# Performance work log

Hardware: AMD Instinct MI355X
Metric: run time of the kernel (lower is better)

## Reference

```python
import jax, jax.numpy as jnp
import numpy as np

N_NODES = 100000


def setup_inputs() -> dict:
    key = jax.random.key(0)
    ks = jax.random.split(key, 7)
    N, F, C, K, E = N_NODES, 64, 32, 3, 1_600_000
    x = jax.random.normal(ks[0], (N, F), dtype=jnp.float32)
    edge_vals = jax.random.uniform(ks[1], (K, E), dtype=jnp.float32)
    W = jax.random.normal(ks[2], (F, C), dtype=jnp.float32) / np.sqrt(F)
    b = jax.random.normal(ks[3], (C,), dtype=jnp.float32) * 0.01
    alpha = jnp.ones((K,), dtype=jnp.float32)
    edge_rows = jax.random.randint(ks[4], (K, E), 0, N, dtype=jnp.int64 if jax.config.jax_enable_x64 else jnp.int32)
    edge_cols = jax.random.randint(ks[5], (K, E), 0, N, dtype=jnp.int64 if jax.config.jax_enable_x64 else jnp.int32)
    return {"x": x, "edge_vals": edge_vals, "W": W, "b": b, "alpha": alpha,
            "edge_rows": edge_rows, "edge_cols": edge_cols}


def reference(x, edge_vals, W, b, alpha, edge_rows, edge_cols):
    # Fused form of: (sum_k alpha[k] * A_k) @ x, then Linear.
    # Per hop k: agg_k[n] = sum_{e: rows[k,e]==n} vals[k,e] * x[cols[k,e]]
    def hop_spmm(vals, rows, cols):
        msg = vals[:, None] * x[cols]                      # [E, F] gather + scale
        return jax.ops.segment_sum(msg, rows, num_segments=N_NODES)  # [N, F]

    agg = jax.vmap(hop_spmm)(edge_vals, edge_rows, edge_cols)  # [K, N, F]
    h = jnp.einsum('k,knf->nf', alpha, agg)                    # weighted hop sum
    return h @ W + b                                           # [N, C]
```

## Files before the change

kernel.cpp:

```cpp
#include <hip/hip_runtime.h>

#define N_NODES 100000
#define F 64
#define C 32
#define KH 3
#define E 1600000
#define NE (KH * E)

#define NSLICE 4
#define SLICEW 25000
#define NKEY (N_NODES * NSLICE)
#define KPB 512
#define NBUCK ((NKEY + KPB - 1) / KPB)
#define CHUNK 4096
#define NCHUNK ((NE + CHUNK - 1) / CHUNK)
#define P2CAP 8192

__global__ __launch_bounds__(256) void gemm_xw(const float* __restrict__ x,
                                               const float* __restrict__ W,
                                               float* __restrict__ y) {
    __shared__ float Ws[F * C];
    for (int i = threadIdx.x; i < F * C; i += 256) Ws[i] = W[i];
    __syncthreads();

    const int g = blockIdx.x * 256 + threadIdx.x;
    if (g >= N_NODES * 2) return;
    const int node = g >> 1;
    const int h = (g & 1) * 16;

    const float4* xp = (const float4*)(x + (size_t)node * F);
    float acc[16];
#pragma unroll
    for (int c = 0; c < 16; c++) acc[c] = 0.f;

#pragma unroll
    for (int i = 0; i < 16; i++) {
        float4 v = xp[i];
        const int f = i * 4;
#pragma unroll
        for (int c = 0; c < 16; c++) {
            acc[c] += v.x * Ws[(f + 0) * C + h + c];
            acc[c] += v.y * Ws[(f + 1) * C + h + c];
            acc[c] += v.z * Ws[(f + 2) * C + h + c];
            acc[c] += v.w * Ws[(f + 3) * C + h + c];
        }
    }

    float4* yo = (float4*)(y + (size_t)node * C + h);
#pragma unroll
    for (int i = 0; i < 4; i++)
        yo[i] = make_float4(acc[4 * i], acc[4 * i + 1], acc[4 * i + 2], acc[4 * i + 3]);
}

__global__ __launch_bounds__(256) void hist_c(const int* __restrict__ rows,
                                              int* __restrict__ hcnt) {
    __shared__ int hh[NBUCK];
    for (int i = threadIdx.x; i < NBUCK; i += 256) hh[i] = 0;
    __syncthreads();
    const int base = blockIdx.x * CHUNK;
#pragma unroll
    for (int j = 0; j < 4; j++) {
        const int e = base + j * 1024 + threadIdx.x * 4;
        if (e + 3 < NE) {
            const int4 r4 = *(const int4*)(rows + e);
            atomicAdd(&hh[r4.x >> 7], 1);
            atomicAdd(&hh[r4.y >> 7], 1);
            atomicAdd(&hh[r4.z >> 7], 1);
            atomicAdd(&hh[r4.w >> 7], 1);
        }
    }
    __syncthreads();
    for (int i = threadIdx.x; i < NBUCK; i += 256) {
        const int cc = hh[i];
        if (cc) atomicAdd(&hcnt[i], cc);
    }
}

__global__ __launch_bounds__(256) void scan_c(const int* __restrict__ hcnt,
                                              int* __restrict__ bstart,
                                              int* __restrict__ bcur,
                                              int* __restrict__ rs_start) {
    __shared__ int sA[1024], sB[1024];
    const int tid = threadIdx.x;
    for (int i = tid; i < 1024; i += 256) sA[i] = (i < NBUCK) ? hcnt[i] : 0;
    __syncthreads();
    int* src = sA;
    int* dst = sB;
    for (int d = 1; d < 1024; d <<= 1) {
        for (int i = tid; i < 1024; i += 256) {
            int v = src[i];
            if (i >= d) v += src[i - d];
            dst[i] = v;
        }
        __syncthreads();
        int* t = src; src = dst; dst = t;
    }
    for (int i = tid; i < NBUCK; i += 256) {
        const int excl = (i == 0) ? 0 : src[i - 1];
        bstart[i] = excl;
        bcur[i] = excl;
    }
    if (tid == 0) {
        bstart[NBUCK] = NE;
        rs_start[NKEY] = NE;
    }
}

__global__ __launch_bounds__(256) void part1_k(const float* __restrict__ vals,
                                               const int* __restrict__ rows,
                                               const int* __restrict__ cols,
                                               const float* __restrict__ alpha,
                                               int* __restrict__ bcur,
                                               int2* __restrict__ edgebuf) {
    __shared__ int sA[1024];
    __shared__ int wtot[4];
    __shared__ int lpos[NBUCK];
    __shared__ int lbase[NBUCK];
    __shared__ int2 stage[CHUNK];
    __shared__ unsigned short sbin[CHUNK];

    const int tid = threadIdx.x;
    const int base = blockIdx.x * CHUNK;

    for (int i = tid; i < 1024; i += 256) sA[i] = 0;
    __syncthreads();

    int kj[16], cj[16];
    float wj[16];
#pragma unroll
    for (int j = 0; j < 4; j++) {
        const int e = base + j * 1024 + tid * 4;
        if (e + 3 < NE) {
            const int4   r4 = *(const int4*)(rows + e);
            const int4   c4 = *(const int4*)(cols + e);
            const float4 v4 = *(const float4*)(vals + e);
            const float ak = alpha[(e >= 2 * E) ? 2 : (e >= E) ? 1 : 0];
            kj[j * 4 + 0] = r4.x * NSLICE + c4.x / SLICEW; cj[j * 4 + 0] = c4.x; wj[j * 4 + 0] = v4.x * ak;
            kj[j * 4 + 1] = r4.y * NSLICE + c4.y / SLICEW; cj[j * 4 + 1] = c4.y; wj[j * 4 + 1] = v4.y * ak;
            kj[j * 4 + 2] = r4.z * NSLICE + c4.z / SLICEW; cj[j * 4 + 2] = c4.z; wj[j * 4 + 2] = v4.z * ak;
            kj[j * 4 + 3] = r4.w * NSLICE + c4.w / SLICEW; cj[j * 4 + 3] = c4.w; wj[j * 4 + 3] = v4.w * ak;
            atomicAdd(&sA[kj[j * 4 + 0] >> 9], 1);
            atomicAdd(&sA[kj[j * 4 + 1] >> 9], 1);
            atomicAdd(&sA[kj[j * 4 + 2] >> 9], 1);
            atomicAdd(&sA[kj[j * 4 + 3] >> 9], 1);
        } else {
            kj[j * 4 + 0] = kj[j * 4 + 1] = kj[j * 4 + 2] = kj[j * 4 + 3] = -1;
        }
    }
    __syncthreads();

    {
        const int lane = tid & 63;
        const int w = tid >> 6;
        const int b4 = tid * 4;
        const int a0 = sA[b4], a1 = sA[b4 + 1], a2 = sA[b4 + 2], a3 = sA[b4 + 3];
        const int l1 = a0 + a1, l2 = l1 + a2, l3 = l2 + a3;
        int sc = l3;
#pragma unroll
        for (int d = 1; d < 64; d <<= 1) {
            int u = __shfl_up(sc, d);
            if (lane >= d) sc += u;
        }
        if (lane == 63) wtot[w] = sc;
        __syncthreads();
        int wb = 0;
#pragma unroll
        for (int q = 0; q < 4; q++)
            if (q < w) wb += wtot[q];
        const int tb = wb + sc - l3;
        sA[b4] = tb + a0; sA[b4 + 1] = tb + l1; sA[b4 + 2] = tb + l2; sA[b4 + 3] = tb + l3;
    }
    __syncthreads();

    for (int i = tid; i < NBUCK; i += 256) {
        const int excl = (i == 0) ? 0 : sA[i - 1];
        const int cnt = sA[i] - excl;
        lpos[i] = excl;
        if (cnt) lbase[i] = atomicAdd(&bcur[i], cnt);
    }
    __syncthreads();

#pragma unroll
    for (int j = 0; j < 16; j++) {
        if (kj[j] >= 0) {
            const int b = kj[j] >> 9;
            const int p = atomicAdd(&lpos[b], 1);
            stage[p] = make_int2(((kj[j] & (KPB - 1)) << 17) | cj[j],
                                 __float_as_int(wj[j]));
            sbin[p] = (unsigned short)b;
        }
    }
    __syncthreads();

    const int total = sA[1023];
    for (int p = tid; p < total; p += 256) {
        const int b = sbin[p];
        const int excl = (b == 0) ? 0 : sA[b - 1];
        edgebuf[lbase[b] + (p - excl)] = stage[p];
    }
}

__global__ __launch_bounds__(512) void part2_k(const int* __restrict__ bstart,
                                               int* __restrict__ rs_start,
                                               int2* __restrict__ edgebuf) {
    __shared__ int2 sstage[P2CAP];
    __shared__ int sh[KPB];
    __shared__ int sg[KPB];
    __shared__ int wtot[8];
    __shared__ int lbin[KPB];

    const int tid = threadIdx.x;
    const int b = blockIdx.x;
    const int bs = bstart[b];
    const int be = bstart[b + 1];
    const int n = be - bs;

    for (int k = tid; k < KPB; k += 512) sh[k] = 0;
    __syncthreads();

    if (n <= P2CAP) {
        for (int i = tid; i < n; i += 512) {
            const int2 e = edgebuf[bs + i];
            sstage[i] = e;
            atomicAdd(&sh[((unsigned)e.x) >> 17], 1);
        }
    }
    __syncthreads();

    {
        const int lane = tid & 63;
        const int w = tid >> 6;
        const int a0 = sh[tid];
        int sc = a0;
#pragma unroll
        for (int d = 1; d < 64; d <<= 1) {
            int u = __shfl_up(sc, d);
            if (lane >= d) sc += u;
        }
        if (lane == 63) wtot[w] = sc;
        __syncthreads();
        int wb = 0;
#pragma unroll
        for (int q = 0; q < 8; q++)
            if (q < w) wb += wtot[q];
        sg[tid] = wb + sc;
    }
    __syncthreads();

    for (int k = tid; k < KPB; k += 512) {
        const int st = bs + ((k == 0) ? 0 : sg[k - 1]);
        lbin[k] = st;
        const int idx = (b << 9) + k;
        if (idx < NKEY) rs_start[idx] = st;
    }
    __syncthreads();

    if (n > P2CAP) return;

    for (int i = tid; i < n; i += 512) {
        const int2 e = sstage[i];
        const int sub = ((unsigned)e.x) >> 17;
        const int pos = atomicAdd(&lbin[sub], 1);
        edgebuf[pos] = e;
    }
}

__global__ __launch_bounds__(256) void gathers9_k(const long long* __restrict__ eb,
                                                  const int* __restrict__ rs_start,
                                                  const float* __restrict__ y,
                                                  const float* __restrict__ bias,
                                                  float* __restrict__ out) {
    const int blk = blockIdx.x;
    const int s = blk & (NSLICE - 1);
    const int row = (blk >> 2) * 8 + (threadIdx.x >> 5);
    const int c = threadIdx.x & 31;
    const int key = row * NSLICE + s;
    const int st = rs_start[key];
    const int en = rs_start[key + 1];

    float acc = (s == 0) ? bias[c] : 0.f;

    int i = st;
    for (; i + 8 <= en; i += 8) {
        const long long l0 = __builtin_nontemporal_load(&eb[i + 0]);
        const long long l1 = __builtin_nontemporal_load(&eb[i + 1]);
        const long long l2 = __builtin_nontemporal_load(&eb[i + 2]);
        const long long l3 = __builtin_nontemporal_load(&eb[i + 3]);
        const long long l4 = __builtin_nontemporal_load(&eb[i + 4]);
        const long long l5 = __builtin_nontemporal_load(&eb[i + 5]);
        const long long l6 = __builtin_nontemporal_load(&eb[i + 6]);
        const long long l7 = __builtin_nontemporal_load(&eb[i + 7]);
        const float y0 = y[(((int)l0) & 0x1FFFF) * C + c];
        const float y1 = y[(((int)l1) & 0x1FFFF) * C + c];
        const float y2 = y[(((int)l2) & 0x1FFFF) * C + c];
        const float y3 = y[(((int)l3) & 0x1FFFF) * C + c];
        const float y4 = y[(((int)l4) & 0x1FFFF) * C + c];
        const float y5 = y[(((int)l5) & 0x1FFFF) * C + c];
        const float y6 = y[(((int)l6) & 0x1FFFF) * C + c];
        const float y7 = y[(((int)l7) & 0x1FFFF) * C + c];
        acc += __int_as_float((int)(l0 >> 32)) * y0;
        acc += __int_as_float((int)(l1 >> 32)) * y1;
        acc += __int_as_float((int)(l2 >> 32)) * y2;
        acc += __int_as_float((int)(l3 >> 32)) * y3;
        acc += __int_as_float((int)(l4 >> 32)) * y4;
        acc += __int_as_float((int)(l5 >> 32)) * y5;
        acc += __int_as_float((int)(l6 >> 32)) * y6;
        acc += __int_as_float((int)(l7 >> 32)) * y7;
    }
    for (; i + 4 <= en; i += 4) {
        const long long l0 = __builtin_nontemporal_load(&eb[i + 0]);
        const long long l1 = __builtin_nontemporal_load(&eb[i + 1]);
        const long long l2 = __builtin_nontemporal_load(&eb[i + 2]);
        const long long l3 = __builtin_nontemporal_load(&eb[i + 3]);
        const float y0 = y[(((int)l0) & 0x1FFFF) * C + c];
        const float y1 = y[(((int)l1) & 0x1FFFF) * C + c];
        const float y2 = y[(((int)l2) & 0x1FFFF) * C + c];
        const float y3 = y[(((int)l3) & 0x1FFFF) * C + c];
        acc += __int_as_float((int)(l0 >> 32)) * y0;
        acc += __int_as_float((int)(l1 >> 32)) * y1;
        acc += __int_as_float((int)(l2 >> 32)) * y2;
        acc += __int_as_float((int)(l3 >> 32)) * y3;
    }
    for (; i < en; i++) {
        const long long l0 = __builtin_nontemporal_load(&eb[i]);
        acc += __int_as_float((int)(l0 >> 32)) * y[(((int)l0) & 0x1FFFF) * C + c];
    }

    unsafeAtomicAdd(out + (size_t)row * C + c, acc);
}

__global__ __launch_bounds__(256) void scatter_edges(
    const float* __restrict__ vals, const int* __restrict__ rows,
    const int* __restrict__ cols, const float* __restrict__ alpha,
    const float* __restrict__ y, float* __restrict__ out_acc) {
    const int t = blockIdx.x * 256 + threadIdx.x;
    const int e = t >> 5;
    const int c = t & 31;
    if (e >= KH * E) return;
    const int k = (e >= 2 * E) ? 2 : (e >= E) ? 1 : 0;
    const float w = vals[e] * alpha[k];
    const float yv = y[(size_t)cols[e] * C + c];
    unsafeAtomicAdd(out_acc + (size_t)rows[e] * C + c, w * yv);
}

__global__ __launch_bounds__(256) void finalize_k(float* __restrict__ out,
                                                  const float* __restrict__ bias) {
    const int idx = (blockIdx.x * 256 + threadIdx.x) * 4;
    if (idx >= N_NODES * C) return;
    const int c0 = idx & (C - 1);
    float4 v = *(float4*)(out + idx);
    v.x += bias[c0 + 0];
    v.y += bias[c0 + 1];
    v.z += bias[c0 + 2];
    v.w += bias[c0 + 3];
    *(float4*)(out + idx) = v;
}

extern "C" void kernel_launch(void* const* d_in, const int* in_sizes, int n_in,
                              void* d_out, int out_size, void* d_ws, size_t ws_size,
                              hipStream_t stream) {
    const float* x         = (const float*)d_in[0];
    const float* edge_vals = (const float*)d_in[1];
    const float* W         = (const float*)d_in[2];
    const float* b         = (const float*)d_in[3];
    const float* alpha     = (const float*)d_in[4];
    const int*   edge_rows = (const int*)d_in[5];
    const int*   edge_cols = (const int*)d_in[6];
    float*       out       = (float*)d_out;

    const size_t offY   = 0;
    const size_t offEB  = (size_t)N_NODES * C * 4;
    const size_t offRS  = offEB + (size_t)NE * 8;
    const size_t offBS  = offRS + (((size_t)(NKEY + 1) * 4 + 255) & ~(size_t)255);
    const size_t offBC  = offBS + (((NBUCK + 1) * 4 + 255) & ~(size_t)255);
    const size_t offHC  = offBC + ((NBUCK * 4 + 255) & ~(size_t)255);
    const size_t need   = offHC + (size_t)NBUCK * 4;

    float* y = (float*)((char*)d_ws + offY);

    gemm_xw<<<(N_NODES * 2 + 255) / 256, 256, 0, stream>>>(x, W, y);

    if (ws_size >= need) {
        int2* edgebuf  = (int2*)((char*)d_ws + offEB);
        int*  rs_start = (int*)((char*)d_ws + offRS);
        int*  bstart   = (int*)((char*)d_ws + offBS);
        int*  bcur     = (int*)((char*)d_ws + offBC);
        int*  hcnt     = (int*)((char*)d_ws + offHC);

        hipMemsetAsync(hcnt, 0, (size_t)NBUCK * 4, stream);
        hipMemsetAsync(out, 0, (size_t)N_NODES * C * sizeof(float), stream);

        hist_c<<<NCHUNK, 256, 0, stream>>>(edge_rows, hcnt);
        scan_c<<<1, 256, 0, stream>>>(hcnt, bstart, bcur, rs_start);
        part1_k<<<NCHUNK, 256, 0, stream>>>(edge_vals, edge_rows, edge_cols,
                                            alpha, bcur, edgebuf);
        part2_k<<<NBUCK, 512, 0, stream>>>(bstart, rs_start, edgebuf);
        gathers9_k<<<(N_NODES / 8) * NSLICE, 256, 0, stream>>>(
            (const long long*)edgebuf, rs_start, y, b, out);
    } else {
        hipMemsetAsync(out, 0, (size_t)N_NODES * C * sizeof(float), stream);
        const long long scatter_threads = (long long)KH * E * C;
        const int scatter_blocks = (int)((scatter_threads + 255) / 256);
        scatter_edges<<<scatter_blocks, 256, 0, stream>>>(
            edge_vals, edge_rows, edge_cols, alpha, y, out);
        finalize_k<<<(N_NODES * C / 4 + 255) / 256, 256, 0, stream>>>(out, b);
    }
}
```

Baseline: 378.6 us.

## Fuse GEMM with row histogram launch and double partition chunk size

The x@W GEMM and the row-bucket histogram are merged into one kernel, with blocks split by index range, so the two independent passes overlap and one launch is removed. The first partition kernel now processes 8192-edge chunks with 512 threads instead of 4096 with 256. This halves the number of global bucket-cursor atomics and makes the write-out runs per bucket longer. The larger shared staging buffer (about 90KB) limits the kernel to fewer resident blocks per CU.

```diff
diff --git a/kernel.cpp b/kernel.cpp
--- a/kernel.cpp
+++ b/kernel.cpp
@@ -12,67 +12,73 @@
 #define NKEY (N_NODES * NSLICE)
 #define KPB 512
 #define NBUCK ((NKEY + KPB - 1) / KPB)
-#define CHUNK 4096
-#define NCHUNK ((NE + CHUNK - 1) / CHUNK)
+#define HCHUNK 4096
+#define NHCHUNK ((NE + HCHUNK - 1) / HCHUNK)
+#define CHUNK1 8192
+#define NCHUNK1 ((NE + CHUNK1 - 1) / CHUNK1)
 #define P2CAP 8192
-
-__global__ __launch_bounds__(256) void gemm_xw(const float* __restrict__ x,
-                                               const float* __restrict__ W,
-                                               float* __restrict__ y) {
-    __shared__ float Ws[F * C];
-    for (int i = threadIdx.x; i < F * C; i += 256) Ws[i] = W[i];
-    __syncthreads();
-
-    const int g = blockIdx.x * 256 + threadIdx.x;
-    if (g >= N_NODES * 2) return;
-    const int node = g >> 1;
-    const int h = (g & 1) * 16;
-
-    const float4* xp = (const float4*)(x + (size_t)node * F);
-    float acc[16];
-#pragma unroll
-    for (int c = 0; c < 16; c++) acc[c] = 0.f;
-
-#pragma unroll
-    for (int i = 0; i < 16; i++) {
-        float4 v = xp[i];
-        const int f = i * 4;
-#pragma unroll
-        for (int c = 0; c < 16; c++) {
-            acc[c] += v.x * Ws[(f + 0) * C + h + c];
-            acc[c] += v.y * Ws[(f + 1) * C + h + c];
-            acc[c] += v.z * Ws[(f + 2) * C + h + c];
-            acc[c] += v.w * Ws[(f + 3) * C + h + c];
-        }
-    }
-
-    float4* yo = (float4*)(y + (size_t)node * C + h);
-#pragma unroll
-    for (int i = 0; i < 4; i++)
-        yo[i] = make_float4(acc[4 * i], acc[4 * i + 1], acc[4 * i + 2], acc[4 * i + 3]);
-}
-
-__global__ __launch_bounds__(256) void hist_c(const int* __restrict__ rows,
-                                              int* __restrict__ hcnt) {
-    __shared__ int hh[NBUCK];
-    for (int i = threadIdx.x; i < NBUCK; i += 256) hh[i] = 0;
-    __syncthreads();
-    const int base = blockIdx.x * CHUNK;
-#pragma unroll
-    for (int j = 0; j < 4; j++) {
-        const int e = base + j * 1024 + threadIdx.x * 4;
-        if (e + 3 < NE) {
-            const int4 r4 = *(const int4*)(rows + e);
-            atomicAdd(&hh[r4.x >> 7], 1);
-            atomicAdd(&hh[r4.y >> 7], 1);
-            atomicAdd(&hh[r4.z >> 7], 1);
-            atomicAdd(&hh[r4.w >> 7], 1);
-        }
-    }
-    __syncthreads();
-    for (int i = threadIdx.x; i < NBUCK; i += 256) {
-        const int cc = hh[i];
-        if (cc) atomicAdd(&hcnt[i], cc);
+#define GEMM_BLOCKS ((N_NODES * 2 + 255) / 256)
+
+__global__ __launch_bounds__(256) void gemm_hist_k(const float* __restrict__ x,
+                                                   const float* __restrict__ W,
+                                                   float* __restrict__ y,
+                                                   const int* __restrict__ rows,
+                                                   int* __restrict__ hcnt) {
+    __shared__ float smem[F * C];
+
+    if (blockIdx.x < GEMM_BLOCKS) {
+        float* Ws = smem;
+        for (int i = threadIdx.x; i < F * C; i += 256) Ws[i] = W[i];
+        __syncthreads();
+
+        const int g = blockIdx.x * 256 + threadIdx.x;
+        if (g >= N_NODES * 2) return;
+        const int node = g >> 1;
+        const int h = (g & 1) * 16;
+
+        const float4* xp = (const float4*)(x + (size_t)node * F);
+        float acc[16];
+#pragma unroll
+        for (int c = 0; c < 16; c++) acc[c] = 0.f;
+
+#pragma unroll
+        for (int i = 0; i < 16; i++) {
+            float4 v = xp[i];
+            const int f = i * 4;
+#pragma unroll
+            for (int c = 0; c < 16; c++) {
+                acc[c] += v.x * Ws[(f + 0) * C + h + c];
+                acc[c] += v.y * Ws[(f + 1) * C + h + c];
+                acc[c] += v.z * Ws[(f + 2) * C + h + c];
+                acc[c] += v.w * Ws[(f + 3) * C + h + c];
+            }
+        }
+
+        float4* yo = (float4*)(y + (size_t)node * C + h);
+#pragma unroll
+        for (int i = 0; i < 4; i++)
+            yo[i] = make_float4(acc[4 * i], acc[4 * i + 1], acc[4 * i + 2], acc[4 * i + 3]);
+    } else {
+        int* hh = (int*)smem;
+        for (int i = threadIdx.x; i < NBUCK; i += 256) hh[i] = 0;
+        __syncthreads();
+        const int base = (blockIdx.x - GEMM_BLOCKS) * HCHUNK;
+#pragma unroll
+        for (int j = 0; j < 4; j++) {
+            const int e = base + j * 1024 + threadIdx.x * 4;
+            if (e + 3 < NE) {
+                const int4 r4 = *(const int4*)(rows + e);
+                atomicAdd(&hh[r4.x >> 7], 1);
+                atomicAdd(&hh[r4.y >> 7], 1);
+                atomicAdd(&hh[r4.z >> 7], 1);
+                atomicAdd(&hh[r4.w >> 7], 1);
+            }
+        }
+        __syncthreads();
+        for (int i = threadIdx.x; i < NBUCK; i += 256) {
+            const int cc = hh[i];
+            if (cc) atomicAdd(&hcnt[i], cc);
+        }
     }
 }
 
@@ -106,30 +112,30 @@
     }
 }
 
-__global__ __launch_bounds__(256) void part1_k(const float* __restrict__ vals,
+__global__ __launch_bounds__(512) void part1_k(const float* __restrict__ vals,
                                                const int* __restrict__ rows,
                                                const int* __restrict__ cols,
                                                const float* __restrict__ alpha,
                                                int* __restrict__ bcur,
                                                int2* __restrict__ edgebuf) {
     __shared__ int sA[1024];
-    __shared__ int wtot[4];
+    __shared__ int wtot[8];
     __shared__ int lpos[NBUCK];
     __shared__ int lbase[NBUCK];
-    __shared__ int2 stage[CHUNK];
-    __shared__ unsigned short sbin[CHUNK];
+    __shared__ int2 stage[CHUNK1];
+    __shared__ unsigned short sbin[CHUNK1];
 
     const int tid = threadIdx.x;
-    const int base = blockIdx.x * CHUNK;
-
-    for (int i = tid; i < 1024; i += 256) sA[i] = 0;
+    const int base = blockIdx.x * CHUNK1;
+
+    for (int i = tid; i < 1024; i += 512) sA[i] = 0;
     __syncthreads();
 
     int kj[16], cj[16];
     float wj[16];
 #pragma unroll
     for (int j = 0; j < 4; j++) {
-        const int e = base + j * 1024 + tid * 4;
+        const int e = base + j * 2048 + tid * 4;
         if (e + 3 < NE) {
             const int4   r4 = *(const int4*)(rows + e);
             const int4   c4 = *(const int4*)(cols + e);
@@ -152,10 +158,10 @@
     {
         const int lane = tid & 63;
         const int w = tid >> 6;
-        const int b4 = tid * 4;
-        const int a0 = sA[b4], a1 = sA[b4 + 1], a2 = sA[b4 + 2], a3 = sA[b4 + 3];
-        const int l1 = a0 + a1, l2 = l1 + a2, l3 = l2 + a3;
-        int sc = l3;
+        const int b2 = tid * 2;
+        const int a0 = sA[b2], a1 = sA[b2 + 1];
+        const int l1 = a0 + a1;
+        int sc = l1;
 #pragma unroll
         for (int d = 1; d < 64; d <<= 1) {
             int u = __shfl_up(sc, d);
@@ -165,14 +171,14 @@
         __syncthreads();
         int wb = 0;
 #pragma unroll
-        for (int q = 0; q < 4; q++)
+        for (int q = 0; q < 8; q++)
             if (q < w) wb += wtot[q];
-        const int tb = wb + sc - l3;
-        sA[b4] = tb + a0; sA[b4 + 1] = tb + l1; sA[b4 + 2] = tb + l2; sA[b4 + 3] = tb + l3;
-    }
-    __syncthreads();
-
-    for (int i = tid; i < NBUCK; i += 256) {
+        const int tb = wb + sc - l1;
+        sA[b2] = tb + a0; sA[b2 + 1] = tb + l1;
+    }
+    __syncthreads();
+
+    for (int i = tid; i < NBUCK; i += 512) {
         const int excl = (i == 0) ? 0 : sA[i - 1];
         const int cnt = sA[i] - excl;
         lpos[i] = excl;
@@ -193,7 +199,7 @@
     __syncthreads();
 
     const int total = sA[1023];
-    for (int p = tid; p < total; p += 256) {
+    for (int p = tid; p < total; p += 512) {
         const int b = sbin[p];
         const int excl = (b == 0) ? 0 : sA[b - 1];
         edgebuf[lbase[b] + (p - excl)] = stage[p];
@@ -343,6 +349,38 @@
     unsafeAtomicAdd(out_acc + (size_t)rows[e] * C + c, w * yv);
 }
 
+__global__ __launch_bounds__(256) void gemm_only_k(const float* __restrict__ x,
+                                                   const float* __restrict__ W,
+                                                   float* __restrict__ y) {
+    __shared__ float Ws[F * C];
+    for (int i = threadIdx.x; i < F * C; i += 256) Ws[i] = W[i];
+    __syncthreads();
+    const int g = blockIdx.x * 256 + threadIdx.x;
+    if (g >= N_NODES * 2) return;
+    const int node = g >> 1;
+    const int h = (g & 1) * 16;
+    const float4* xp = (const float4*)(x + (size_t)node * F);
+    float acc[16];
+#pragma unroll
+    for (int c = 0; c < 16; c++) acc[c] = 0.f;
+#pragma unroll
+    for (int i = 0; i < 16; i++) {
+        float4 v = xp[i];
+        const int f = i * 4;
+#pragma unroll
+        for (int c = 0; c < 16; c++) {
+            acc[c] += v.x * Ws[(f + 0) * C + h + c];
+            acc[c] += v.y * Ws[(f + 1) * C + h + c];
+            acc[c] += v.z * Ws[(f + 2) * C + h + c];
+            acc[c] += v.w * Ws[(f + 3) * C + h + c];
+        }
+    }
+    float4* yo = (float4*)(y + (size_t)node * C + h);
+#pragma unroll
+    for (int i = 0; i < 4; i++)
+        yo[i] = make_float4(acc[4 * i], acc[4 * i + 1], acc[4 * i + 2], acc[4 * i + 3]);
+}
+
 __global__ __launch_bounds__(256) void finalize_k(float* __restrict__ out,
                                                   const float* __restrict__ bias) {
     const int idx = (blockIdx.x * 256 + threadIdx.x) * 4;
@@ -378,8 +416,6 @@
 
     float* y = (float*)((char*)d_ws + offY);
 
-    gemm_xw<<<(N_NODES * 2 + 255) / 256, 256, 0, stream>>>(x, W, y);
-
     if (ws_size >= need) {
         int2* edgebuf  = (int2*)((char*)d_ws + offEB);
         int*  rs_start = (int*)((char*)d_ws + offRS);
@@ -390,14 +426,16 @@
         hipMemsetAsync(hcnt, 0, (size_t)NBUCK * 4, stream);
         hipMemsetAsync(out, 0, (size_t)N_NODES * C * sizeof(float), stream);
 
-        hist_c<<<NCHUNK, 256, 0, stream>>>(edge_rows, hcnt);
+        gemm_hist_k<<<GEMM_BLOCKS + NHCHUNK, 256, 0, stream>>>(
+            x, W, y, edge_rows, hcnt);
         scan_c<<<1, 256, 0, stream>>>(hcnt, bstart, bcur, rs_start);
-        part1_k<<<NCHUNK, 256, 0, stream>>>(edge_vals, edge_rows, edge_cols,
-                                            alpha, bcur, edgebuf);
+        part1_k<<<NCHUNK1, 512, 0, stream>>>(edge_vals, edge_rows, edge_cols,
+                                             alpha, bcur, edgebuf);
         part2_k<<<NBUCK, 512, 0, stream>>>(bstart, rs_start, edgebuf);
         gathers9_k<<<(N_NODES / 8) * NSLICE, 256, 0, stream>>>(
             (const long long*)edgebuf, rs_start, y, b, out);
     } else {
+        gemm_only_k<<<GEMM_BLOCKS, 256, 0, stream>>>(x, W, y);
         hipMemsetAsync(out, 0, (size_t)N_NODES * C * sizeof(float), stream);
         const long long scatter_threads = (long long)KH * E * C;
         const int scatter_blocks = (int)((scatter_threads + 255) / 256);
```

Result: faster. 355.4 us (-6.1%).
